# Optimization experiments

Measured on AMD Instinct MI355X. Metric: run time of the kernel, lower is better.

## Reference

```python
import jax, jax.numpy as jnp
import numpy as np

DIM = 768
HEADS = 12
HEAD_DIM = DIM // HEADS
SCALE = HEAD_DIM ** -0.5


def setup_inputs() -> dict:
    key = jax.random.key(0)
    k1, k2, k3, k4 = jax.random.split(key, 4)
    x = jax.random.normal(k1, (1, 4096, DIM), dtype=jnp.float32)
    # qkv: Linear(dim, 3*dim), bias=False
    W_qkv = jax.random.normal(k2, (DIM, 3 * DIM), dtype=jnp.float32) * (DIM ** -0.5)
    # proj: Linear(dim, dim) with bias
    W_proj = jax.random.normal(k3, (DIM, DIM), dtype=jnp.float32) * (DIM ** -0.5)
    b_proj = jax.random.normal(k4, (DIM,), dtype=jnp.float32) * 0.01
    return {"x": x, "W_qkv": W_qkv, "W_proj": W_proj, "b_proj": b_proj}


def reference(x, W_qkv, W_proj, b_proj):
    b, n, d = x.shape
    qkv = x @ W_qkv                                  # [b, n, 3d]
    q, k, v = jnp.split(qkv, 3, axis=-1)             # each [b, n, d]
    # split heads: [b, n, (h hd)] -> [b, h, n, hd]
    def heads(t):
        return t.reshape(b, n, HEADS, HEAD_DIM).transpose(0, 2, 1, 3)
    q, k, v = heads(q) * SCALE, heads(k), heads(v)
    sim = jnp.einsum('bhid,bhjd->bhij', q, k)        # [b, h, n, n] -- full score matrix
    attn = jax.nn.softmax(sim, axis=-1)
    out = jnp.einsum('bhij,bhjd->bhid', attn, v)     # [b, h, n, hd]
    out = out.transpose(0, 2, 1, 3).reshape(b, n, d)  # merge heads
    return out @ W_proj + b_proj
```

## Files before the change

kernel.cpp:

```cpp
#include <hip/hip_runtime.h>
#include <math.h>

#define TOKENS 4096
#define DMODEL 768
#define NHEADS 12
#define HDIM   64
#define QKV_N  2304
#define ATTN_SCALE 0.125f
#define QSCALE_LOG2E (0.125f * 1.44269504088896340736f)

typedef __attribute__((ext_vector_type(8))) short bf16x8;
typedef __attribute__((ext_vector_type(4))) float floatx4;

__device__ __forceinline__ ushort f2bf(float f) {
    union { float f; unsigned u; } cv; cv.f = f;
    unsigned u = cv.u;
    u += 0x7fffu + ((u >> 16) & 1u);
    return (ushort)(u >> 16);
}

__device__ __forceinline__ unsigned cvt_pk_bf16(float a, float b) {
    unsigned r;
    asm("v_cvt_pk_bf16_f32 %0, %1, %2" : "=v"(r) : "v"(a), "v"(b));
    return r;
}

__device__ __forceinline__ void gl2lds16(const ushort* g, ushort* l) {
    __builtin_amdgcn_global_load_lds(
        (const __attribute__((address_space(1))) void*)g,
        (__attribute__((address_space(3))) void*)l, 16, 0, 0);
}

__device__ __forceinline__ bf16x8 frag(const ushort* ls, int row, int chunk) {
    return *(const bf16x8*)(ls + row * 64 + ((chunk ^ (row & 7)) * 8));
}

__global__ __launch_bounds__(256) void prep_kernel(
    const float* __restrict__ x, const float* __restrict__ Wqkv,
    const float* __restrict__ Wproj, ushort* __restrict__ Xb,
    ushort* __restrict__ WqkvT, ushort* __restrict__ WprojT)
{
    __shared__ ushort tile[32][33];
    const int bid = blockIdx.x;
    const int tid = threadIdx.x;

    if (bid < 3072) {
        const int i = bid * 256 + tid;
        const float4 v = ((const float4*)x)[i];
        ushort4 h;
        h.x = f2bf(v.x); h.y = f2bf(v.y); h.z = f2bf(v.z); h.w = f2bf(v.w);
        ((ushort4*)Xb)[i] = h;
        return;
    }

    const float* in; ushort* out; int C, bx, by;
    if (bid < 3072 + 1728) {
        const int b = bid - 3072;
        in = Wqkv; out = WqkvT; C = QKV_N;
        bx = b % 72; by = b / 72;
    } else {
        const int b = bid - 4800;
        in = Wproj; out = WprojT; C = DMODEL;
        bx = b % 24; by = b / 24;
    }
    const int R  = DMODEL;
    const int tx = tid & 31;
    const int ty8 = tid >> 5;
    const int c0 = bx * 32;
    const int r0 = by * 32;
    #pragma unroll
    for (int p = 0; p < 4; ++p) {
        const int r = ty8 + p * 8;
        tile[r][tx] = f2bf(in[(size_t)(r0 + r) * C + c0 + tx]);
    }
    __syncthreads();
    #pragma unroll
    for (int p = 0; p < 4; ++p) {
        const int c = ty8 + p * 8;
        out[(size_t)(c0 + c) * R + r0 + tx] = tile[tx][c];
    }
}

template<int NT>
__device__ __forceinline__ void gemm_body_async(
    const ushort* __restrict__ A, const ushort* __restrict__ Bt, int K,
    int m0, int n0, floatx4 acc[4][NT], ushort* ls)
{
    ushort* lsA = ls;
    ushort* lsB = ls + 8192;

    const int tid  = threadIdx.x;
    const int lane = tid & 63;
    const int wave = tid >> 6;
    const int wm = wave >> 1, wn = wave & 1;
    const int quad = lane >> 4, l16 = lane & 15;

    const int lrow = lane >> 3;
    const int csw  = ((lane & 7) ^ lrow) * 8;

    const ushort* gA = A  + (size_t)(m0 + wave * 32 + lrow) * K + csw;
    const ushort* gB = Bt + (size_t)(n0 + wave * NT * 8 + lrow) * K + csw;
    ushort* lA = lsA + (wave * 32) * 64;
    ushort* lB = lsB + (wave * NT * 8) * 64;

    for (int k0 = 0; k0 < K; k0 += 64) {
        __syncthreads();
        #pragma unroll
        for (int p = 0; p < 4; ++p)
            gl2lds16(gA + (size_t)p * 8 * K + k0, lA + p * 8 * 64);
        #pragma unroll
        for (int p = 0; p < NT; ++p)
            gl2lds16(gB + (size_t)p * 8 * K + k0, lB + p * 8 * 64);
        __syncthreads();

        #pragma unroll
        for (int ks = 0; ks < 2; ++ks) {
            bf16x8 af[4], bfr[NT];
            #pragma unroll
            for (int mt = 0; mt < 4; ++mt)
                af[mt] = frag(lsA, wm * 64 + mt * 16 + l16, ks * 4 + quad);
            #pragma unroll
            for (int nt = 0; nt < NT; ++nt)
                bfr[nt] = frag(lsB, wn * NT * 16 + nt * 16 + l16, ks * 4 + quad);
            #pragma unroll
            for (int mt = 0; mt < 4; ++mt)
                #pragma unroll
                for (int nt = 0; nt < NT; ++nt)
                    acc[mt][nt] = __builtin_amdgcn_mfma_f32_16x16x32_bf16(
                        af[mt], bfr[nt], acc[mt][nt], 0, 0, 0);
        }
    }
}

__global__ __launch_bounds__(256) void gemm_qkv_mfma(
    const ushort* __restrict__ Xb, const ushort* __restrict__ Wt,
    ushort* __restrict__ Qb, ushort* __restrict__ Kb, ushort* __restrict__ Vt)
{
    __shared__ __align__(16) ushort ls[17408];
    const int lin = blockIdx.x + blockIdx.y * 18;
    const int w   = (lin & 7) * 72 + (lin >> 3);
    const int m0  = (w / 18) * 128;
    const int n0  = (w % 18) * 128;

    floatx4 acc[4][4] = {};
    gemm_body_async<4>(Xb, Wt, DMODEL, m0, n0, acc, ls);

    const int tid  = threadIdx.x;
    const int lane = tid & 63;
    const int wave = tid >> 6;
    const int wm = wave >> 1, wn = wave & 1;
    const int quad = lane >> 4, l16 = lane & 15;

    if (n0 < 2 * DMODEL) {
        const float scale = (n0 < DMODEL) ? QSCALE_LOG2E : 1.0f;
        ushort* outp = (n0 < DMODEL) ? Qb : Kb;
        const int colg = (n0 < DMODEL) ? n0 : n0 - DMODEL;
        __syncthreads();
        #pragma unroll
        for (int mt = 0; mt < 4; ++mt)
            #pragma unroll
            for (int nt = 0; nt < 4; ++nt) {
                const int row = wm * 64 + mt * 16 + quad * 4;
                const int col = wn * 64 + nt * 16 + l16;
                #pragma unroll
                for (int r = 0; r < 4; ++r)
                    ls[(row + r) * 136 + col] = f2bf(acc[mt][nt][r] * scale);
            }
        __syncthreads();
        #pragma unroll
        for (int p2 = 0; p2 < 8; ++p2) {
            const int row = (tid >> 4) + p2 * 16;
            const int c8  = (tid & 15) * 8;
            *(uint4*)(outp + (size_t)(m0 + row) * DMODEL + colg + c8) =
                *(const uint4*)(ls + row * 136 + c8);
        }
    } else {
        const int hd0 = n0 - 2 * DMODEL;
        __syncthreads();
        #pragma unroll
        for (int mt = 0; mt < 4; ++mt)
            #pragma unroll
            for (int nt = 0; nt < 4; ++nt) {
                const int hd  = wn * 64 + nt * 16 + l16;
                const int tok = wm * 64 + mt * 16 + quad * 4;
                #pragma unroll
                for (int r = 0; r < 4; ++r)
                    ls[hd * 136 + tok + r] = f2bf(acc[mt][nt][r]);
            }
        __syncthreads();
        #pragma unroll
        for (int p2 = 0; p2 < 8; ++p2) {
            const int row = (tid >> 4) + p2 * 16;
            const int c8  = (tid & 15) * 8;
            *(uint4*)(Vt + (size_t)(hd0 + row) * TOKENS + m0 + c8) =
                *(const uint4*)(ls + row * 136 + c8);
        }
    }
}

__global__ __launch_bounds__(256) void gemm_proj_mfma(
    const ushort* __restrict__ Ab, const ushort* __restrict__ Wt,
    const float* __restrict__ bias, float* __restrict__ out)
{
    __shared__ __align__(16) ushort ls[12288];
    const int lin = blockIdx.x + blockIdx.y * 12;
    const int w   = (lin & 7) * 48 + (lin >> 3);
    const int m0  = (w / 12) * 128;
    const int n0  = (w % 12) * 64;

    floatx4 acc[4][2] = {};
    gemm_body_async<2>(Ab, Wt, DMODEL, m0, n0, acc, ls);

    const int lane = threadIdx.x & 63;
    const int wave = threadIdx.x >> 6;
    const int wm = wave >> 1, wn = wave & 1;
    const int quad = lane >> 4, l16 = lane & 15;
    const int row0 = m0 + wm * 64 + quad * 4;
    const int col0 = n0 + wn * 32;

    #pragma unroll
    for (int nt = 0; nt < 2; ++nt) {
        const int col = col0 + nt * 16 + l16;
        const float bv = bias[col];
        #pragma unroll
        for (int mt = 0; mt < 4; ++mt)
            #pragma unroll
            for (int r = 0; r < 4; ++r)
                out[(size_t)(row0 + mt * 16 + r) * DMODEL + col] =
                    acc[mt][nt][r] + bv;
    }
}

__global__ __launch_bounds__(256, 3) void attn_mfma_kernel(
    const ushort* __restrict__ Qb, const ushort* __restrict__ Kb,
    const ushort* __restrict__ Vt, ushort* __restrict__ attn_out)
{
    __shared__ __align__(16) ushort lds[25728];

    const int tid  = threadIdx.x;
    const int wave = tid >> 6;
    const int lane = tid & 63;
    const int quad = lane >> 4;
    const int l16  = lane & 15;

    const int lin = blockIdx.x + blockIdx.y * 64;
    const int wsw = (lin & 7) * 96 + (lin >> 3);
    const int h   = wsw >> 6;
    const int i0  = (wsw & 63) * 64;

    bf16x8 qf[4][2];
    #pragma unroll
    for (int jt = 0; jt < 4; ++jt) {
        const ushort* qb = Qb + (size_t)(i0 + jt * 16 + l16) * DMODEL + h * HDIM;
        qf[jt][0] = *(const bf16x8*)(qb + quad * 8);
        qf[jt][1] = *(const bf16x8*)(qb + 32 + quad * 8);
    }

    bf16x8 ones;
    #pragma unroll
    for (int i = 0; i < 8; ++i) ones[i] = (short)0x3F80;

    floatx4 O[4][4] = {};
    floatx4 Ol[4]   = {};

    ushort* wls = lds + wave * 6144;

    const int lrow8 = lane >> 3;
    const int csw8  = ((lane & 7) ^ lrow8) * 8;
    const ushort* gK0 = Kb + (size_t)(wave * 16 + lrow8) * DMODEL + h * HDIM + csw8;
    const ushort* gK1 = gK0 + (size_t)8 * DMODEL;

    const ushort* gV0 = Vt + (size_t)(h * HDIM + (lane >> 1)) * TOKENS
                           + wave * 16 + (((lane & 1) ^ ((lane >> 3) & 1)) * 8);
    const ushort* gV1 = gV0 + (size_t)32 * TOKENS;

    const int vo = ((quad >> 1) ^ ((l16 >> 2) & 1)) * 8 + (quad & 1) * 4;

    union { bf16x8 v; unsigned u[4]; } pa[4];

    gl2lds16(gK0, wls);
    gl2lds16(gK1, wls + 512);
    gl2lds16(gV0, wls + 2048);
    gl2lds16(gV1, wls + 2048 + 512);

    for (int u = 0; u < 32; ++u) {
        const int s0 = (u & 1) << 1;
        ushort* Kc0 = wls;
        ushort* Kc1 = wls + 1024;
        ushort* V0  = wls + 2048 + s0 * 1024;
        ushort* V1  = wls + 2048 + (s0 + 1) * 1024;
        ushort* Vn  = wls + 2048 + ((s0 + 2) & 3) * 1024;

        {
            const size_t t1 = (size_t)(2 * u + 1) * 64;
            gl2lds16(gK0 + t1 * DMODEL, Kc1);
            gl2lds16(gK1 + t1 * DMODEL, Kc1 + 512);
            gl2lds16(gV0 + t1, V1);
            gl2lds16(gV1 + t1, V1 + 512);
        }
        asm volatile("s_waitcnt vmcnt(4)" ::: "memory");

        {
            const bf16x8 a0 = frag(Kc0, l16, quad);
            const bf16x8 a1 = frag(Kc0, l16, 4 + quad);
            __builtin_amdgcn_s_setprio(1);
            #pragma unroll
            for (int jt = 0; jt < 4; ++jt) {
                floatx4 s = {0.f, 0.f, 0.f, 0.f};
                s = __builtin_amdgcn_mfma_f32_16x16x32_bf16(a0, qf[jt][0], s, 0, 0, 0);
                s = __builtin_amdgcn_mfma_f32_16x16x32_bf16(a1, qf[jt][1], s, 0, 0, 0);
                pa[jt].u[0] = cvt_pk_bf16(__builtin_amdgcn_exp2f(s[0]),
                                          __builtin_amdgcn_exp2f(s[1]));
                pa[jt].u[1] = cvt_pk_bf16(__builtin_amdgcn_exp2f(s[2]),
                                          __builtin_amdgcn_exp2f(s[3]));
            }
            __builtin_amdgcn_s_setprio(0);
        }

        if (u < 31) {
            const size_t t2 = (size_t)(2 * u + 2) * 64;
            gl2lds16(gK0 + t2 * DMODEL, Kc0);
            gl2lds16(gK1 + t2 * DMODEL, Kc0 + 512);
            gl2lds16(gV0 + t2, Vn);
            gl2lds16(gV1 + t2, Vn + 512);
            asm volatile("s_waitcnt vmcnt(4)" ::: "memory");
        } else {
            asm volatile("s_waitcnt vmcnt(0)" ::: "memory");
        }

        {
            const bf16x8 a0 = frag(Kc1, l16, quad);
            const bf16x8 a1 = frag(Kc1, l16, 4 + quad);
            __builtin_amdgcn_s_setprio(1);
            #pragma unroll
            for (int jt = 0; jt < 4; ++jt) {
                floatx4 s = {0.f, 0.f, 0.f, 0.f};
                s = __builtin_amdgcn_mfma_f32_16x16x32_bf16(a0, qf[jt][0], s, 0, 0, 0);
                s = __builtin_amdgcn_mfma_f32_16x16x32_bf16(a1, qf[jt][1], s, 0, 0, 0);
                pa[jt].u[2] = cvt_pk_bf16(__builtin_amdgcn_exp2f(s[0]),
                                          __builtin_amdgcn_exp2f(s[1]));
                pa[jt].u[3] = cvt_pk_bf16(__builtin_amdgcn_exp2f(s[2]),
                                          __builtin_amdgcn_exp2f(s[3]));
            }
            __builtin_amdgcn_s_setprio(0);
        }

        __builtin_amdgcn_s_setprio(1);
        #pragma unroll
        for (int nt = 0; nt < 4; ++nt) {
            const int ro = (nt * 16 + l16) * 16 + vo;
            union { bf16x8 v; uint2 d[2]; } vu;
            vu.d[0] = *(const uint2*)(V0 + ro);
            vu.d[1] = *(const uint2*)(V1 + ro);
            #pragma unroll
            for (int jt = 0; jt < 4; ++jt)
                O[jt][nt] = __builtin_amdgcn_mfma_f32_16x16x32_bf16(
                    pa[jt].v, vu.v, O[jt][nt], 0, 0, 0);
        }
        #pragma unroll
        for (int jt = 0; jt < 4; ++jt)
            Ol[jt] = __builtin_amdgcn_mfma_f32_16x16x32_bf16(
                pa[jt].v, ones, Ol[jt], 0, 0, 0);
        __builtin_amdgcn_s_setprio(0);
    }

    __syncthreads();
    float* Of  = (float*)lds;
    float* Olf = ((float*)lds) + 3 * 64 * 66;
    if (wave != 0) {
        const int rg = (wave - 1) * 64 * 66;
        #pragma unroll
        for (int jt = 0; jt < 4; ++jt) {
            #pragma unroll
            for (int nt = 0; nt < 4; ++nt)
                #pragma unroll
                for (int r = 0; r < 4; ++r)
                    Of[rg + (jt * 16 + quad * 4 + r) * 66 + nt * 16 + l16] = O[jt][nt][r];
            if (l16 == 0) {
                #pragma unroll
                for (int r = 0; r < 4; ++r)
                    Olf[(wave - 1) * 64 + jt * 16 + quad * 4 + r] = Ol[jt][r];
            }
        }
    }
    __syncthreads();
    if (wave == 0) {
        #pragma unroll
        for (int jt = 0; jt < 4; ++jt) {
            const int qr = jt * 16 + quad * 4;
            float linv[4];
            #pragma unroll
            for (int r = 0; r < 4; ++r) {
                const float l = Ol[jt][r] + Olf[qr + r] + Olf[64 + qr + r]
                              + Olf[128 + qr + r];
                linv[r] = __builtin_amdgcn_rcpf(l);
            }
            #pragma unroll
            for (int nt = 0; nt < 4; ++nt) {
                const int d = h * HDIM + nt * 16 + l16;
                #pragma unroll
                for (int r = 0; r < 4; ++r) {
                    const float o = O[jt][nt][r]
                        + Of[(qr + r) * 66 + nt * 16 + l16]
                        + Of[64 * 66 + (qr + r) * 66 + nt * 16 + l16]
                        + Of[2 * 64 * 66 + (qr + r) * 66 + nt * 16 + l16];
                    attn_out[(size_t)(i0 + qr + r) * DMODEL + d] = f2bf(o * linv[r]);
                }
            }
        }
    }
}

extern "C" void kernel_launch(void* const* d_in, const int* in_sizes, int n_in,
                              void* d_out, int out_size, void* d_ws, size_t ws_size,
                              hipStream_t stream)
{
    const float* x     = (const float*)d_in[0];
    const float* Wqkv  = (const float*)d_in[1];
    const float* Wproj = (const float*)d_in[2];
    const float* bproj = (const float*)d_in[3];
    float* out = (float*)d_out;

    ushort* Xb     = (ushort*)d_ws;
    ushort* WqkvT  = Xb    + (size_t)TOKENS * DMODEL;
    ushort* WprojT = WqkvT + (size_t)QKV_N * DMODEL;
    ushort* Qb     = WprojT + (size_t)DMODEL * DMODEL;
    ushort* Kb     = Qb    + (size_t)TOKENS * DMODEL;
    ushort* Vt     = Kb    + (size_t)TOKENS * DMODEL;
    ushort* attn   = Vt    + (size_t)TOKENS * DMODEL;

    prep_kernel<<<dim3(5376), 256, 0, stream>>>(
        x, Wqkv, Wproj, Xb, WqkvT, WprojT);

    gemm_qkv_mfma<<<dim3(QKV_N / 128, TOKENS / 128), 256, 0, stream>>>(
        Xb, WqkvT, Qb, Kb, Vt);

    attn_mfma_kernel<<<dim3(TOKENS / 64, NHEADS), 256, 0, stream>>>(
        Qb, Kb, Vt, attn);

    gemm_proj_mfma<<<dim3(DMODEL / 64, TOKENS / 128), 256, 0, stream>>>(
        attn, WprojT, bproj, out);
}
```

Baseline: 186.3 us.

## Double-buffer LDS tiles in QKV and projection GEMMs to overlap loads with MFMA

Replaces the single-buffer GEMM main loop with a two-phase ping-pong scheme. The next K-tile's global-to-LDS async loads are issued before the MFMA work on the current tile, and only one barrier is kept per iteration. This is meant to hide global memory latency behind compute in both GEMM kernels. LDS use per block roughly doubles, which may lower occupancy. Correctness also depends on the async loads having finished before the barrier.

```diff
diff --git a/kernel.cpp b/kernel.cpp
--- a/kernel.cpp
+++ b/kernel.cpp
@@ -82,12 +82,11 @@
 }
 
 template<int NT>
-__device__ __forceinline__ void gemm_body_async(
+__device__ __forceinline__ void gemm_body_2ph(
     const ushort* __restrict__ A, const ushort* __restrict__ Bt, int K,
     int m0, int n0, floatx4 acc[4][NT], ushort* ls)
 {
-    ushort* lsA = ls;
-    ushort* lsB = ls + 8192;
+    const int BUF = 8192 + 2048 * NT;
 
     const int tid  = threadIdx.x;
     const int lane = tid & 63;
@@ -100,19 +99,34 @@
 
     const ushort* gA = A  + (size_t)(m0 + wave * 32 + lrow) * K + csw;
     const ushort* gB = Bt + (size_t)(n0 + wave * NT * 8 + lrow) * K + csw;
-    ushort* lA = lsA + (wave * 32) * 64;
-    ushort* lB = lsB + (wave * NT * 8) * 64;
-
-    for (int k0 = 0; k0 < K; k0 += 64) {
-        __syncthreads();
-        #pragma unroll
-        for (int p = 0; p < 4; ++p)
-            gl2lds16(gA + (size_t)p * 8 * K + k0, lA + p * 8 * 64);
-        #pragma unroll
-        for (int p = 0; p < NT; ++p)
-            gl2lds16(gB + (size_t)p * 8 * K + k0, lB + p * 8 * 64);
-        __syncthreads();
-
+    const int lAoff = (wave * 32) * 64;
+    const int lBoff = 8192 + (wave * NT * 8) * 64;
+
+    #pragma unroll
+    for (int p = 0; p < 4; ++p)
+        gl2lds16(gA + (size_t)p * 8 * K, ls + lAoff + p * 8 * 64);
+    #pragma unroll
+    for (int p = 0; p < NT; ++p)
+        gl2lds16(gB + (size_t)p * 8 * K, ls + lBoff + p * 8 * 64);
+    __syncthreads();
+
+    const int NK = K / 64;
+    for (int t = 0; t < NK; ++t) {
+        ushort* cb = ls + (t & 1) * BUF;
+        ushort* nb = ls + ((t + 1) & 1) * BUF;
+
+        if (t + 1 < NK) {
+            const int k1 = (t + 1) * 64;
+            #pragma unroll
+            for (int p = 0; p < 4; ++p)
+                gl2lds16(gA + (size_t)p * 8 * K + k1, nb + lAoff + p * 8 * 64);
+            #pragma unroll
+            for (int p = 0; p < NT; ++p)
+                gl2lds16(gB + (size_t)p * 8 * K + k1, nb + lBoff + p * 8 * 64);
+        }
+
+        const ushort* lsA = cb;
+        const ushort* lsB = cb + 8192;
         #pragma unroll
         for (int ks = 0; ks < 2; ++ks) {
             bf16x8 af[4], bfr[NT];
@@ -129,6 +143,8 @@
                     acc[mt][nt] = __builtin_amdgcn_mfma_f32_16x16x32_bf16(
                         af[mt], bfr[nt], acc[mt][nt], 0, 0, 0);
         }
+
+        __syncthreads();
     }
 }
 
@@ -136,14 +152,14 @@
     const ushort* __restrict__ Xb, const ushort* __restrict__ Wt,
     ushort* __restrict__ Qb, ushort* __restrict__ Kb, ushort* __restrict__ Vt)
 {
-    __shared__ __align__(16) ushort ls[17408];
+    __shared__ __align__(16) ushort ls[32768];
     const int lin = blockIdx.x + blockIdx.y * 18;
     const int w   = (lin & 7) * 72 + (lin >> 3);
     const int m0  = (w / 18) * 128;
     const int n0  = (w % 18) * 128;
 
     floatx4 acc[4][4] = {};
-    gemm_body_async<4>(Xb, Wt, DMODEL, m0, n0, acc, ls);
+    gemm_body_2ph<4>(Xb, Wt, DMODEL, m0, n0, acc, ls);
 
     const int tid  = threadIdx.x;
     const int lane = tid & 63;
@@ -202,14 +218,14 @@
     const ushort* __restrict__ Ab, const ushort* __restrict__ Wt,
     const float* __restrict__ bias, float* __restrict__ out)
 {
-    __shared__ __align__(16) ushort ls[12288];
+    __shared__ __align__(16) ushort ls[24576];
     const int lin = blockIdx.x + blockIdx.y * 12;
     const int w   = (lin & 7) * 48 + (lin >> 3);
     const int m0  = (w / 12) * 128;
     const int n0  = (w % 12) * 64;
 
     floatx4 acc[4][2] = {};
-    gemm_body_async<2>(Ab, Wt, DMODEL, m0, n0, acc, ls);
+    gemm_body_2ph<2>(Ab, Wt, DMODEL, m0, n0, acc, ls);
 
     const int lane = threadIdx.x & 63;
     const int wave = threadIdx.x >> 6;
```

After: 181.4 us. 1.03x faster.
